# Optimization experiments

Measured on AMD Instinct MI355X. Metric: run time of the kernel, lower is better.

Reference implementation:

```python
import jax, jax.numpy as jnp
import numpy as np

H, E, D, S, B = 16, 1024, 64, 2048, 4  # heads, emb, head_size, seq_len, batch

def setup_inputs() -> dict:
    key = jax.random.key(0)
    ks = jax.random.split(key, 9)
    sc_e = 1.0 / np.sqrt(E)
    sc_hd = 1.0 / np.sqrt(H * D)
    return {
        "x":  jax.random.normal(ks[0], (B, S, E), dtype=jnp.float32),
        # per-head q/k/v projection weights, stacked: [H, E, D]
        "Wq": jax.random.uniform(ks[1], (H, E, D), jnp.float32, -sc_e, sc_e),
        "Wk": jax.random.uniform(ks[2], (H, E, D), jnp.float32, -sc_e, sc_e),
        "Wv": jax.random.uniform(ks[3], (H, E, D), jnp.float32, -sc_e, sc_e),
        "bq": jax.random.uniform(ks[4], (H, D), jnp.float32, -sc_e, sc_e),
        "bk": jax.random.uniform(ks[5], (H, D), jnp.float32, -sc_e, sc_e),
        "bv": jax.random.uniform(ks[6], (H, D), jnp.float32, -sc_e, sc_e),
        # output projection: Linear(H*D -> E)
        "Wo": jax.random.uniform(ks[7], (H * D, E), jnp.float32, -sc_hd, sc_hd),
        "bo": jax.random.uniform(ks[8], (E,), jnp.float32, -sc_hd, sc_hd),
    }

def reference(x, Wq, Wk, Wv, bq, bk, bv, Wo, bo):
    b, s, e = x.shape
    # batched per-head projections: [B, H, S, D]
    q = jnp.einsum("bse,hed->bhsd", x, Wq) + bq[None, :, None, :]
    k = jnp.einsum("bse,hed->bhsd", x, Wk) + bk[None, :, None, :]
    v = jnp.einsum("bse,hed->bhsd", x, Wv) + bv[None, :, None, :]
    scale = 1.0 / jnp.sqrt(jnp.asarray(q.shape[-1], q.dtype))
    scores = jnp.einsum("bhqd,bhkd->bhqk", q, k) * scale  # [B,H,S,S]
    causal = jnp.tril(jnp.ones((s, s), dtype=bool))
    scores = jnp.where(causal[None, None], scores, jnp.asarray(-jnp.inf, scores.dtype))
    attn = jax.nn.softmax(scores, axis=-1)
    heads = jnp.einsum("bhqk,bhkd->bhqd", attn, v)  # [B,H,S,D]
    concat = heads.transpose(0, 2, 1, 3).reshape(b, s, -1)  # [B,S,H*D]
    return concat @ Wo + bo  # dropout is identity at inference
```

## Files before the change

kernel.cpp:

```cpp
#include <hip/hip_runtime.h>
#include <hip/hip_bf16.h>

#define H_ 16
#define E_ 1024
#define D_ 64
#define S_ 2048
#define B_ 4
#define M_ (B_ * S_)

typedef __bf16 bf16_t;
typedef __bf16 bf16x8 __attribute__((ext_vector_type(8)));
typedef __bf16 bf16x4 __attribute__((ext_vector_type(4)));
typedef float f32x4 __attribute__((ext_vector_type(4)));

typedef __attribute__((address_space(1))) unsigned int gu32;
typedef __attribute__((address_space(3))) unsigned int lu32;

__device__ __forceinline__ f32x4 mfma16(bf16x8 a, bf16x8 b, f32x4 c) {
  return __builtin_amdgcn_mfma_f32_16x16x32_bf16(a, b, c, 0, 0, 0);
}
__device__ __forceinline__ void gl2lds16(const bf16_t* g, bf16_t* l) {
  __builtin_amdgcn_global_load_lds((const gu32*)g, (lu32*)l, 16, 0, 0);
}

__device__ __forceinline__ int detect_f32(const unsigned short* __restrict__ xu) {
  int lane = threadIdx.x & 63;
  int cnt = 0;
  for (int i = 0; i < 4; ++i) {
    unsigned short v = xu[(lane * 4 + i) * 2];
    cnt += __popcll(__ballot(((v >> 7) & 0xFF) >= 0xC0));
  }
  return cnt > 16;
}

__global__ __launch_bounds__(256) void convert_x(
    const void* __restrict__ src, bf16_t* __restrict__ dst,
    int* __restrict__ flag, long n) {
  const int f32 = detect_f32((const unsigned short*)src);
  if (blockIdx.x == 0 && threadIdx.x == 0) { flag[0] = f32; flag[1] = 0; }
  long i = ((long)blockIdx.x * 256 + threadIdx.x) * 8;
  if (i >= n) return;
  bf16x8 v;
  if (f32) {
    const float* s = (const float*)src;
    for (int j = 0; j < 8; ++j) v[j] = (bf16_t)s[i + j];
  } else {
    v = *(const bf16x8*)((const bf16_t*)src + i);
  }
  *(bf16x8*)(dst + i) = v;
}

__global__ __launch_bounds__(256) void transpose_k(
    const void* __restrict__ src_, bf16_t* __restrict__ dst,
    const int* __restrict__ flag, int K, int N, long sStride, long dStride) {
  __shared__ __align__(16) bf16_t tile[64][72];
  const int f32 = *flag;
  dst += (long)blockIdx.z * dStride;
  const int tk = blockIdx.x * 64, tn = blockIdx.y * 64;
  const int t = threadIdx.x;
  for (int i = 0; i < 2; ++i) {
    int c = t + i * 256;
    int r = c >> 3, col = (c & 7) * 8;
    if (f32) {
      const float* s = (const float*)src_ + (long)blockIdx.z * sStride;
      const float* p = &s[(long)(tk + r) * N + tn + col];
      for (int j = 0; j < 8; ++j) tile[r][col + j] = (bf16_t)p[j];
    } else {
      const bf16_t* s = (const bf16_t*)src_ + (long)blockIdx.z * sStride;
      *(bf16x8*)&tile[r][col] = *(const bf16x8*)&s[(long)(tk + r) * N + tn + col];
    }
  }
  __syncthreads();
  for (int i = 0; i < 2; ++i) {
    int c = t + i * 256;
    int r = c >> 3, col = (c & 7) * 8;
    bf16x8 v;
    for (int j = 0; j < 8; ++j) v[j] = tile[col + j][r];
    *(bf16x8*)&dst[(long)(tn + r) * K + tk + col] = v;
  }
}

__global__ __launch_bounds__(256) void transpose_qkv(
    const void* __restrict__ s0, const void* __restrict__ s1,
    const void* __restrict__ s2,
    bf16_t* __restrict__ d0, bf16_t* __restrict__ d1, bf16_t* __restrict__ d2,
    const int* __restrict__ flag) {
  __shared__ __align__(16) bf16_t tile[64][72];
  const int f32 = *flag;
  const int which = blockIdx.z >> 4, h = blockIdx.z & 15;
  const void* src_ = which == 0 ? s0 : (which == 1 ? s1 : s2);
  bf16_t* dst = (which == 0 ? d0 : (which == 1 ? d1 : d2)) + (long)h * E_ * D_;
  const long sOff = (long)h * E_ * D_;
  const int tk = blockIdx.x * 64;
  const int t = threadIdx.x;
  for (int i = 0; i < 2; ++i) {
    int c = t + i * 256;
    int r = c >> 3, col = (c & 7) * 8;
    if (f32) {
      const float* s = (const float*)src_ + sOff;
      const float* p = &s[(long)(tk + r) * D_ + col];
      for (int j = 0; j < 8; ++j) tile[r][col + j] = (bf16_t)p[j];
    } else {
      const bf16_t* s = (const bf16_t*)src_ + sOff;
      *(bf16x8*)&tile[r][col] = *(const bf16x8*)&s[(long)(tk + r) * D_ + col];
    }
  }
  __syncthreads();
  for (int i = 0; i < 2; ++i) {
    int c = t + i * 256;
    int r = c >> 3, col = (c & 7) * 8;
    bf16x8 v;
    for (int j = 0; j < 8; ++j) v[j] = tile[col + j][r];
    *(bf16x8*)&dst[(long)r * E_ + tk + col] = v;
  }
}

__global__ __launch_bounds__(256) void gemm_qkv(
    const bf16_t* __restrict__ A,
    const bf16_t* __restrict__ Bt0, const bf16_t* __restrict__ Bt1,
    const bf16_t* __restrict__ Bt2,
    const void* __restrict__ b0, const void* __restrict__ b1,
    const void* __restrict__ b2,
    bf16_t* __restrict__ C0, bf16_t* __restrict__ C1, bf16_t* __restrict__ C2,
    const int* __restrict__ flag) {
  constexpr int K = 1024;
  __shared__ __align__(16) bf16_t As[128 * 32];
  __shared__ __align__(16) bf16_t Bs[128 * 32];
  const int z = blockIdx.z;
  const bf16_t* Bt = z == 0 ? Bt0 : (z == 1 ? Bt1 : Bt2);
  const void* bias = z == 0 ? b0 : (z == 1 ? b1 : b2);
  bf16_t* C = z == 0 ? C0 : (z == 1 ? C1 : C2);
  const int t = threadIdx.x;
  const int wave = t >> 6, lane = t & 63;
  const int quad = lane >> 4, l16 = lane & 15;
  const int m0 = blockIdx.x * 128, n0 = blockIdx.y * 128;
  const int wm = (wave & 1) * 64, wn = (wave >> 1) * 64;
  const int swz = (l16 >> 1) & 3;
  f32x4 acc[4][4] = {};

  for (int kt = 0; kt < K; kt += 32) {
    __syncthreads();
    for (int i = 0; i < 2; ++i) {
      int c = i * 256 + wave * 64 + lane;
      int row = c >> 2;
      int srcc = (c & 3) ^ ((c >> 3) & 3);
      int dst = (i * 256 + wave * 64) * 8;
      gl2lds16(&A[(long)(m0 + row) * K + kt + srcc * 8], &As[dst]);
      gl2lds16(&Bt[(long)(n0 + row) * K + kt + srcc * 8], &Bs[dst]);
    }
    __syncthreads();
    bf16x8 af[4], bfr[4];
    for (int mt = 0; mt < 4; ++mt)
      af[mt] = *(const bf16x8*)&As[(wm + mt * 16 + l16) * 32 + ((quad ^ swz) << 3)];
    for (int nt = 0; nt < 4; ++nt)
      bfr[nt] = *(const bf16x8*)&Bs[(wn + nt * 16 + l16) * 32 + ((quad ^ swz) << 3)];
    for (int mt = 0; mt < 4; ++mt)
      for (int nt = 0; nt < 4; ++nt)
        acc[mt][nt] = mfma16(af[mt], bfr[nt], acc[mt][nt]);
  }
  const int f32io = *flag;
  for (int nt = 0; nt < 4; ++nt) {
    int n = n0 + wn + nt * 16 + l16;
    float bv = f32io ? ((const float*)bias)[n] : (float)((const bf16_t*)bias)[n];
    int h = n >> 6, d = n & 63;
    for (int mt = 0; mt < 4; ++mt)
      for (int r = 0; r < 4; ++r) {
        int m = m0 + wm + mt * 16 + quad * 4 + r;
        int b = m >> 11, s = m & (S_ - 1);
        C[(((long)(b * H_ + h)) * S_ + s) * D_ + d] = (bf16_t)(acc[mt][nt][r] + bv);
      }
  }
}

__global__ __launch_bounds__(256) void gemm_out(
    const bf16_t* __restrict__ A, const bf16_t* __restrict__ Bt,
    const void* __restrict__ bias, void* __restrict__ C,
    const int* __restrict__ flag) {
  constexpr int K = 1024, N = 1024;
  __shared__ __align__(16) bf16_t As[128 * 32];
  __shared__ __align__(16) bf16_t Bs[128 * 32];
  const int t = threadIdx.x;
  const int wave = t >> 6, lane = t & 63;
  const int quad = lane >> 4, l16 = lane & 15;
  const int m0 = blockIdx.x * 128, n0 = blockIdx.y * 128;
  const int wm = (wave & 1) * 64, wn = (wave >> 1) * 64;
  const int swz = (l16 >> 1) & 3;
  const int f32io = *flag;
  f32x4 acc[4][4] = {};

  for (int kt = 0; kt < K; kt += 32) {
    __syncthreads();
    for (int i = 0; i < 2; ++i) {
      int c = i * 256 + wave * 64 + lane;
      int row = c >> 2;
      int srcc = (c & 3) ^ ((c >> 3) & 3);
      int dst = (i * 256 + wave * 64) * 8;
      int m = m0 + row, kk = kt + srcc * 8;
      int b = m >> 11, s = m & (S_ - 1);
      int h = kk >> 6, d = kk & 63;
      gl2lds16(&A[(((long)(b * H_ + h)) * S_ + s) * D_ + d], &As[dst]);
      gl2lds16(&Bt[(long)(n0 + row) * K + kt + srcc * 8], &Bs[dst]);
    }
    __syncthreads();
    bf16x8 af[4], bfr[4];
    for (int mt = 0; mt < 4; ++mt)
      af[mt] = *(const bf16x8*)&As[(wm + mt * 16 + l16) * 32 + ((quad ^ swz) << 3)];
    for (int nt = 0; nt < 4; ++nt)
      bfr[nt] = *(const bf16x8*)&Bs[(wn + nt * 16 + l16) * 32 + ((quad ^ swz) << 3)];
    for (int mt = 0; mt < 4; ++mt)
      for (int nt = 0; nt < 4; ++nt)
        acc[mt][nt] = mfma16(af[mt], bfr[nt], acc[mt][nt]);
  }
  for (int mt = 0; mt < 4; ++mt) {
    for (int nt = 0; nt < 4; ++nt) {
      int n = n0 + wn + nt * 16 + l16;
      float bv = f32io ? ((const float*)bias)[n] : (float)((const bf16_t*)bias)[n];
      for (int r = 0; r < 4; ++r) {
        int m = m0 + wm + mt * 16 + quad * 4 + r;
        float v = acc[mt][nt][r] + bv;
        if (f32io) ((float*)C)[(long)m * N + n] = v;
        else       ((bf16_t*)C)[(long)m * N + n] = (bf16_t)v;
      }
    }
  }
}

__global__ __launch_bounds__(256) void attn_k(
    bf16_t* QO,
    const bf16_t* __restrict__ Kg_,
    const bf16_t* __restrict__ Vtg_) {
  __shared__ __align__(16) bf16_t Ks[64 * 64];
  __shared__ __align__(16) bf16_t Vs[64 * 64];
  __shared__ __align__(16) bf16_t Pq[4][32 * 72];
  const int t = threadIdx.x;
  const int wave = t >> 6, lane = t & 63;
  const int quad = lane >> 4, l16 = lane & 15;
  const int bid = blockIdx.x;
  const int qb = 15 - (bid >> 6);
  const int bh = bid & 63;
  const long base = (long)bh * S_ * D_;
  bf16_t* Qg = QO + base;
  const bf16_t* Kg = Kg_ + base;
  const bf16_t* Vt = Vtg_ + base;
  const int q0 = qb * 128, qrl = wave * 32;
  const int rot = ((lane & 7) - (lane >> 3)) & 7;

  bf16x8 qf[2][2];
  for (int n = 0; n < 2; ++n) {
    long row = q0 + qrl + n * 16 + l16;
    bf16x8 a = *(const bf16x8*)&Qg[row * D_ + quad * 8];
    bf16x8 b = *(const bf16x8*)&Qg[row * D_ + 32 + quad * 8];
    for (int j = 0; j < 8; ++j) {
      a[j] = (bf16_t)((float)a[j] * 0.18033688f);
      b[j] = (bf16_t)((float)b[j] * 0.18033688f);
    }
    qf[n][0] = a; qf[n][1] = b;
  }
  bf16x8 ones;
  for (int j = 0; j < 8; ++j) ones[j] = (bf16_t)1.0f;
  f32x4 o_acc[2][4] = {};
  f32x4 lacc[2] = {};

  const int nkt = 2 * qb + 2;
  for (int kt = 0; kt < nkt; ++kt) {
    __syncthreads();
    for (int i = 0; i < 2; ++i) {
      int c = wave * 2 + i;
      gl2lds16(&Kg[(long)(kt * 64 + c * 8 + (lane >> 3)) * D_ + rot * 8],
               &Ks[c * 512]);
      gl2lds16(&Vt[(long)(c * 8 + (lane >> 3)) * S_ + kt * 64 + rot * 8],
               &Vs[c * 512]);
    }
    __syncthreads();

    if (kt * 64 > q0 + qrl + 31) continue;

    f32x4 sc[2][4];
    for (int mt = 0; mt < 4; ++mt) {
      int krow = mt * 16 + l16;
      bf16x8 kf0 = *(const bf16x8*)&Ks[krow * 64 + (((quad + krow) & 7) << 3)];
      bf16x8 kf1 = *(const bf16x8*)&Ks[krow * 64 + (((quad + 4 + krow) & 7) << 3)];
      for (int n = 0; n < 2; ++n) {
        f32x4 z = {0.f, 0.f, 0.f, 0.f};
        z = mfma16(kf0, qf[n][0], z);
        z = mfma16(kf1, qf[n][1], z);
        sc[n][mt] = z;
      }
    }
    if (kt * 64 + 63 > q0 + qrl) {
      for (int n = 0; n < 2; ++n) {
        int qr = q0 + qrl + n * 16 + l16;
        for (int mt = 0; mt < 4; ++mt)
          for (int r = 0; r < 4; ++r) {
            int kc = kt * 64 + mt * 16 + quad * 4 + r;
            if (kc > qr) sc[n][mt][r] = -1e30f;
          }
      }
    }
    for (int n = 0; n < 2; ++n)
      for (int mt = 0; mt < 4; ++mt) {
        bf16x4 pb;
        for (int r = 0; r < 4; ++r)
          pb[r] = (bf16_t)__builtin_amdgcn_exp2f(sc[n][mt][r]);
        *(bf16x4*)&Pq[wave][(n * 16 + l16) * 72 + mt * 16 + quad * 4] = pb;
      }
    bf16x8 pf[2][2];
    for (int m = 0; m < 2; ++m) {
      pf[m][0] = *(const bf16x8*)&Pq[wave][(m * 16 + l16) * 72 + quad * 8];
      pf[m][1] = *(const bf16x8*)&Pq[wave][(m * 16 + l16) * 72 + 32 + quad * 8];
    }
    for (int m = 0; m < 2; ++m) {
      lacc[m] = mfma16(pf[m][0], ones, lacc[m]);
      lacc[m] = mfma16(pf[m][1], ones, lacc[m]);
    }
    for (int dt = 0; dt < 4; ++dt) {
      int drow = dt * 16 + l16;
      bf16x8 vf0 = *(const bf16x8*)&Vs[drow * 64 + (((quad + drow) & 7) << 3)];
      bf16x8 vf1 = *(const bf16x8*)&Vs[drow * 64 + (((quad + 4 + drow) & 7) << 3)];
      for (int m = 0; m < 2; ++m) {
        o_acc[m][dt] = mfma16(pf[m][0], vf0, o_acc[m][dt]);
        o_acc[m][dt] = mfma16(pf[m][1], vf1, o_acc[m][dt]);
      }
    }
  }
  for (int m = 0; m < 2; ++m)
    for (int r = 0; r < 4; ++r) {
      float inv = 1.0f / lacc[m][r];
      long qg = q0 + qrl + m * 16 + quad * 4 + r;
      for (int dt = 0; dt < 4; ++dt)
        Qg[qg * D_ + dt * 16 + l16] = (bf16_t)(o_acc[m][dt][r] * inv);
    }
}

extern "C" void kernel_launch(void* const* d_in, const int* in_sizes, int n_in,
                              void* d_out, int out_size, void* d_ws, size_t ws_size,
                              hipStream_t stream) {
  (void)in_sizes; (void)n_in; (void)out_size; (void)ws_size;
  const void* x  = d_in[0];
  const void* Wq = d_in[1];
  const void* Wk = d_in[2];
  const void* Wv = d_in[3];
  const void* bq = d_in[4];
  const void* bk = d_in[5];
  const void* bv = d_in[6];
  const void* Wo = d_in[7];
  const void* bo = d_in[8];

  char* base = (char*)d_ws;
  int* flag = (int*)base;
  bf16_t* p = (bf16_t*)(base + 16);
  bf16_t* xb_ = p; p += (size_t)M_ * E_;
  bf16_t* qo_ = p; p += (size_t)B_ * H_ * S_ * D_;
  bf16_t* kb_ = p; p += (size_t)B_ * H_ * S_ * D_;
  bf16_t* vb_ = p; p += (size_t)B_ * H_ * S_ * D_;
  bf16_t* wqt = p; p += (size_t)H_ * D_ * E_;
  bf16_t* wkt = p; p += (size_t)H_ * D_ * E_;
  bf16_t* wvt = p; p += (size_t)H_ * D_ * E_;
  bf16_t* wot = p; p += (size_t)E_ * E_;

  convert_x<<<(M_ * E_) / (256 * 8), 256, 0, stream>>>(x, xb_, flag, (long)M_ * E_);

  transpose_qkv<<<dim3(16, 1, 48), 256, 0, stream>>>(Wq, Wk, Wv, wqt, wkt, wvt, flag);
  transpose_k<<<dim3(16, 16, 1), 256, 0, stream>>>(Wo, wot, flag, E_, E_, 0, 0);

  gemm_qkv<<<dim3(M_ / 128, 8, 3), 256, 0, stream>>>(
      xb_, wqt, wkt, wvt, bq, bk, bv, qo_, kb_, vb_, flag);

  transpose_k<<<dim3(S_ / 64, 1, B_ * H_), 256, 0, stream>>>(
      vb_, xb_, flag + 1, S_, D_, (long)S_ * D_, (long)S_ * D_);

  attn_k<<<dim3(1024), 256, 0, stream>>>(qo_, kb_, xb_);

  gemm_out<<<dim3(M_ / 128, 8), 256, 0, stream>>>(qo_, wot, bo, d_out, flag);
}
```

Baseline: 289.5 us.

## Replace QKV and output GEMMs with 256-row, 8-wave double-buffered pipelined kernel

After: 303.2 us. +4.7%, slower.

```diff
diff --git a/kernel.cpp b/kernel.cpp
--- a/kernel.cpp
+++ b/kernel.cpp
@@ -22,6 +22,8 @@
 __device__ __forceinline__ void gl2lds16(const bf16_t* g, bf16_t* l) {
   __builtin_amdgcn_global_load_lds((const gu32*)g, (lu32*)l, 16, 0, 0);
 }
+
+#define BAR() asm volatile("s_barrier" ::: "memory")
 
 __device__ __forceinline__ int detect_f32(const unsigned short* __restrict__ xu) {
   int lane = threadIdx.x & 63;
@@ -115,111 +117,161 @@
   }
 }
 
-__global__ __launch_bounds__(256) void gemm_qkv(
-    const bf16_t* __restrict__ A,
-    const bf16_t* __restrict__ Bt0, const bf16_t* __restrict__ Bt1,
-    const bf16_t* __restrict__ Bt2,
-    const void* __restrict__ b0, const void* __restrict__ b1,
-    const void* __restrict__ b2,
-    bf16_t* __restrict__ C0, bf16_t* __restrict__ C1, bf16_t* __restrict__ C2,
+template <int NBF, int KIND>
+__global__ __launch_bounds__(512, 2) void gemm8(
+    const bf16_t* __restrict__ A, const bf16_t* __restrict__ Bt,
+    const void* __restrict__ bias0, const void* __restrict__ bias1,
+    const void* __restrict__ bias2,
+    bf16_t* __restrict__ Cq, void* __restrict__ Cout,
     const int* __restrict__ flag) {
-  constexpr int K = 1024;
-  __shared__ __align__(16) bf16_t As[128 * 32];
-  __shared__ __align__(16) bf16_t Bs[128 * 32];
-  const int z = blockIdx.z;
-  const bf16_t* Bt = z == 0 ? Bt0 : (z == 1 ? Bt1 : Bt2);
-  const void* bias = z == 0 ? b0 : (z == 1 ? b1 : b2);
-  bf16_t* C = z == 0 ? C0 : (z == 1 ? C1 : C2);
+  __shared__ __align__(16) bf16_t LA[2 * 256 * 64];
+  __shared__ __align__(16) bf16_t LB[2 * NBF * 64 * 64];
   const int t = threadIdx.x;
   const int wave = t >> 6, lane = t & 63;
   const int quad = lane >> 4, l16 = lane & 15;
-  const int m0 = blockIdx.x * 128, n0 = blockIdx.y * 128;
-  const int wm = (wave & 1) * 64, wn = (wave >> 1) * 64;
-  const int swz = (l16 >> 1) & 3;
-  f32x4 acc[4][4] = {};
-
-  for (int kt = 0; kt < K; kt += 32) {
-    __syncthreads();
-    for (int i = 0; i < 2; ++i) {
-      int c = i * 256 + wave * 64 + lane;
-      int row = c >> 2;
-      int srcc = (c & 3) ^ ((c >> 3) & 3);
-      int dst = (i * 256 + wave * 64) * 8;
-      gl2lds16(&A[(long)(m0 + row) * K + kt + srcc * 8], &As[dst]);
-      gl2lds16(&Bt[(long)(n0 + row) * K + kt + srcc * 8], &Bs[dst]);
-    }
-    __syncthreads();
-    bf16x8 af[4], bfr[4];
-    for (int mt = 0; mt < 4; ++mt)
-      af[mt] = *(const bf16x8*)&As[(wm + mt * 16 + l16) * 32 + ((quad ^ swz) << 3)];
-    for (int nt = 0; nt < 4; ++nt)
-      bfr[nt] = *(const bf16x8*)&Bs[(wn + nt * 16 + l16) * 32 + ((quad ^ swz) << 3)];
-    for (int mt = 0; mt < 4; ++mt)
-      for (int nt = 0; nt < 4; ++nt)
-        acc[mt][nt] = mfma16(af[mt], bfr[nt], acc[mt][nt]);
-  }
-  const int f32io = *flag;
-  for (int nt = 0; nt < 4; ++nt) {
-    int n = n0 + wn + nt * 16 + l16;
-    float bv = f32io ? ((const float*)bias)[n] : (float)((const bf16_t*)bias)[n];
-    int h = n >> 6, d = n & 63;
-    for (int mt = 0; mt < 4; ++mt)
-      for (int r = 0; r < 4; ++r) {
-        int m = m0 + wm + mt * 16 + quad * 4 + r;
-        int b = m >> 11, s = m & (S_ - 1);
-        C[(((long)(b * H_ + h)) * S_ + s) * D_ + d] = (bf16_t)(acc[mt][nt][r] + bv);
-      }
-  }
-}
-
-__global__ __launch_bounds__(256) void gemm_out(
-    const bf16_t* __restrict__ A, const bf16_t* __restrict__ Bt,
-    const void* __restrict__ bias, void* __restrict__ C,
-    const int* __restrict__ flag) {
-  constexpr int K = 1024, N = 1024;
-  __shared__ __align__(16) bf16_t As[128 * 32];
-  __shared__ __align__(16) bf16_t Bs[128 * 32];
-  const int t = threadIdx.x;
-  const int wave = t >> 6, lane = t & 63;
-  const int quad = lane >> 4, l16 = lane & 15;
-  const int m0 = blockIdx.x * 128, n0 = blockIdx.y * 128;
-  const int wm = (wave & 1) * 64, wn = (wave >> 1) * 64;
-  const int swz = (l16 >> 1) & 3;
-  const int f32io = *flag;
-  f32x4 acc[4][4] = {};
-
-  for (int kt = 0; kt < K; kt += 32) {
-    __syncthreads();
-    for (int i = 0; i < 2; ++i) {
-      int c = i * 256 + wave * 64 + lane;
-      int row = c >> 2;
-      int srcc = (c & 3) ^ ((c >> 3) & 3);
-      int dst = (i * 256 + wave * 64) * 8;
-      int m = m0 + row, kk = kt + srcc * 8;
+  const int wm = (wave >> 2) * 128;
+  const int wn = (wave & 3) * (NBF * 16);
+  constexpr int CPX = (KIND == 0) ? 64 : 32;
+  const int bid = blockIdx.x;
+  const int wg = (bid & 7) * CPX + (bid >> 3);
+  const int m0 = (wg & 31) * 256;
+  const int n0 = (wg >> 5) * (NBF * 64);
+
+  f32x4 acc[8][NBF] = {};
+  bf16x8 af[4], bfr[NBF];
+
+  const int sr = lane >> 3;
+  const int sj = ((lane & 7) ^ sr) << 3;
+  auto stA = [&](int u, int tt) {
+    bf16_t* l = &LA[(tt & 1) * 16384 + u * 4096 + wave * 512];
+    if constexpr (KIND == 0) {
+      gl2lds16(&A[(long)(m0 + u * 64 + wave * 8 + sr) * 1024 + (tt & 15) * 64 + sj], l);
+    } else {
+      int m = m0 + u * 64 + wave * 8 + sr;
       int b = m >> 11, s = m & (S_ - 1);
-      int h = kk >> 6, d = kk & 63;
-      gl2lds16(&A[(((long)(b * H_ + h)) * S_ + s) * D_ + d], &As[dst]);
-      gl2lds16(&Bt[(long)(n0 + row) * K + kt + srcc * 8], &Bs[dst]);
-    }
-    __syncthreads();
-    bf16x8 af[4], bfr[4];
-    for (int mt = 0; mt < 4; ++mt)
-      af[mt] = *(const bf16x8*)&As[(wm + mt * 16 + l16) * 32 + ((quad ^ swz) << 3)];
-    for (int nt = 0; nt < 4; ++nt)
-      bfr[nt] = *(const bf16x8*)&Bs[(wn + nt * 16 + l16) * 32 + ((quad ^ swz) << 3)];
-    for (int mt = 0; mt < 4; ++mt)
-      for (int nt = 0; nt < 4; ++nt)
-        acc[mt][nt] = mfma16(af[mt], bfr[nt], acc[mt][nt]);
-  }
-  for (int mt = 0; mt < 4; ++mt) {
-    for (int nt = 0; nt < 4; ++nt) {
-      int n = n0 + wn + nt * 16 + l16;
-      float bv = f32io ? ((const float*)bias)[n] : (float)((const bf16_t*)bias)[n];
-      for (int r = 0; r < 4; ++r) {
-        int m = m0 + wm + mt * 16 + quad * 4 + r;
-        float v = acc[mt][nt][r] + bv;
-        if (f32io) ((float*)C)[(long)m * N + n] = v;
-        else       ((bf16_t*)C)[(long)m * N + n] = (bf16_t)v;
+      gl2lds16(&A[(((long)(b * H_ + (tt & 15))) * S_ + s) * D_ + sj], l);
+    }
+  };
+  auto stB = [&](int u, int tt) {
+    bf16_t* l = &LB[(tt & 1) * (NBF * 4096) + u * 4096 + wave * 512];
+    gl2lds16(&Bt[(long)(n0 + u * 64 + wave * 8 + sr) * 1024 + (tt & 15) * 64 + sj], l);
+  };
+
+  auto rdA = [&](int buf, int i, int kk) {
+    int R = wm + i * 16 + l16;
+    return *(const bf16x8*)&LA[buf * 16384 + R * 64 + (((kk * 4 + quad) ^ (R & 7)) << 3)];
+  };
+  auto rdB = [&](int buf, int j, int kk) {
+    int R = wn + j * 16 + l16;
+    return *(const bf16x8*)&LB[buf * (NBF * 4096) + R * 64 + (((kk * 4 + quad) ^ (R & 7)) << 3)];
+  };
+  auto quarter = [&](int buf, int kk, int up, bool rb) {
+#pragma unroll
+    for (int i = 0; i < 4; ++i) af[i] = rdA(buf, up * 4 + i, kk);
+    if (rb) {
+#pragma unroll
+      for (int j = 0; j < NBF; ++j) bfr[j] = rdB(buf, j, kk);
+    }
+    __builtin_amdgcn_s_setprio(1);
+#pragma unroll
+    for (int i = 0; i < 4; ++i)
+#pragma unroll
+      for (int j = 0; j < NBF; ++j)
+        acc[up * 4 + i][j] = mfma16(bfr[j], af[i], acc[up * 4 + i][j]);
+    __builtin_amdgcn_s_setprio(0);
+  };
+
+  stB(0, 0); stB(1, 0);
+  if constexpr (NBF == 3) stB(2, 0);
+  stA(0, 0); stA(1, 0); stA(2, 0); stA(3, 0);
+  stB(0, 1);
+
+#pragma unroll 1
+  for (int it = 0; it < 8; ++it) {
+    const int T1 = 2 * it + 1, T2 = 2 * it + 2, T3 = 2 * it + 3;
+    stB(1, T1);
+    if constexpr (NBF == 3) stB(2, T1);
+    if constexpr (NBF == 3) asm volatile("s_waitcnt vmcnt(3)" ::: "memory");
+    else                    asm volatile("s_waitcnt vmcnt(2)" ::: "memory");
+    BAR();
+    quarter(0, 0, 0, true);
+    BAR();
+    stA(0, T1); stA(1, T1);
+    BAR();
+    quarter(0, 0, 1, false);
+    BAR();
+    stA(2, T1); stA(3, T1);
+    BAR();
+    quarter(0, 1, 0, true);
+    BAR();
+    stB(0, T2);
+    BAR();
+    quarter(0, 1, 1, false);
+    BAR();
+    stB(1, T2);
+    if constexpr (NBF == 3) stB(2, T2);
+    if constexpr (NBF == 3) asm volatile("s_waitcnt vmcnt(3)" ::: "memory");
+    else                    asm volatile("s_waitcnt vmcnt(2)" ::: "memory");
+    BAR();
+    quarter(1, 0, 0, true);
+    BAR();
+    stA(0, T2); stA(1, T2);
+    BAR();
+    quarter(1, 0, 1, false);
+    BAR();
+    stA(2, T2); stA(3, T2);
+    BAR();
+    quarter(1, 1, 0, true);
+    BAR();
+    stB(0, T3);
+    BAR();
+    quarter(1, 1, 1, false);
+    BAR();
+  }
+
+  const int f32io = flag[0];
+  if constexpr (KIND == 0) {
+#pragma unroll
+    for (int i = 0; i < 8; ++i) {
+      const int m = m0 + wm + i * 16 + l16;
+      const int b = m >> 11, s = m & (S_ - 1);
+#pragma unroll
+      for (int j = 0; j < NBF; ++j) {
+        const int n = n0 + wn + j * 16 + quad * 4;
+        const int which = n >> 10, nin = n & 1023;
+        const int h = nin >> 6, d = nin & 63;
+        const void* bp = which == 0 ? bias0 : (which == 1 ? bias1 : bias2);
+        bf16x4 o;
+#pragma unroll
+        for (int r = 0; r < 4; ++r) {
+          float bv = f32io ? ((const float*)bp)[nin + r]
+                           : (float)((const bf16_t*)bp)[nin + r];
+          o[r] = (bf16_t)(acc[i][j][r] + bv);
+        }
+        *(bf16x4*)&Cq[(long)which * (B_ * H_ * S_ * D_) +
+                      (((long)(b * H_ + h)) * S_ + s) * D_ + d] = o;
+      }
+    }
+  } else {
+#pragma unroll
+    for (int i = 0; i < 8; ++i) {
+      const long m = m0 + wm + i * 16 + l16;
+#pragma unroll
+      for (int j = 0; j < NBF; ++j) {
+        const int n = n0 + wn + j * 16 + quad * 4;
+        if (f32io) {
+          f32x4 o;
+#pragma unroll
+          for (int r = 0; r < 4; ++r)
+            o[r] = acc[i][j][r] + ((const float*)bias0)[n + r];
+          *(f32x4*)&((float*)Cout)[m * 1024 + n] = o;
+        } else {
+          bf16x4 o;
+#pragma unroll
+          for (int r = 0; r < 4; ++r)
+            o[r] = (bf16_t)(acc[i][j][r] + (float)((const bf16_t*)bias0)[n + r]);
+          *(bf16x4*)&((bf16_t*)Cout)[m * 1024 + n] = o;
+        }
       }
     }
   }
@@ -363,13 +415,14 @@
   transpose_qkv<<<dim3(16, 1, 48), 256, 0, stream>>>(Wq, Wk, Wv, wqt, wkt, wvt, flag);
   transpose_k<<<dim3(16, 16, 1), 256, 0, stream>>>(Wo, wot, flag, E_, E_, 0, 0);
 
-  gemm_qkv<<<dim3(M_ / 128, 8, 3), 256, 0, stream>>>(
-      xb_, wqt, wkt, wvt, bq, bk, bv, qo_, kb_, vb_, flag);
+  gemm8<3, 0><<<dim3(512), 512, 0, stream>>>(
+      xb_, wqt, bq, bk, bv, qo_, nullptr, flag);
 
   transpose_k<<<dim3(S_ / 64, 1, B_ * H_), 256, 0, stream>>>(
       vb_, xb_, flag + 1, S_, D_, (long)S_ * D_, (long)S_ * D_);
 
   attn_k<<<dim3(1024), 256, 0, stream>>>(qo_, kb_, xb_);
 
-  gemm_out<<<dim3(M_ / 128, 8), 256, 0, stream>>>(qo_, wot, bo, d_out, flag);
-}
+  gemm8<2, 1><<<dim3(256), 512, 0, stream>>>(
+      qo_, wot, bo, nullptr, nullptr, nullptr, d_out, flag);
+}
```
